# Performance work log

Measured on AMD Instinct MI355X. Metric: run time of the kernel, lower is better.

The kernel has to match this reference:

```python
import math
import jax, jax.numpy as jnp
import numpy as np

B, S, D = 1, 2048, 4096
H, KV, Dh = 32, 8, 128          # query heads, kv heads, head dim
G = H // KV                      # GQA group size
THETA = 10000.0
FACTOR = 4.0
BETA_FAST, BETA_SLOW, ORIG_MAX = 32, 1, 32768


def _yarn_rope_cache(seq_len):
    """YaRN-scaled RoPE cos/sin cache, matching YaRNRotaryEmbedding._build_cache."""
    inv_freq = 1.0 / (THETA ** (np.arange(0, Dh, 2, dtype=np.float32) / Dh))
    low = ORIG_MAX / (2 * math.pi * BETA_SLOW)
    high = ORIG_MAX / (2 * math.pi * BETA_FAST)
    freq = 1.0 / inv_freq
    smooth = np.clip((freq - low) / (high - low), 0.0, 1.0)
    inv_freq = (1.0 - smooth) * inv_freq + smooth * (inv_freq / FACTOR)
    t = np.arange(seq_len, dtype=np.float32)
    freqs = np.outer(t, inv_freq)                 # [S, Dh/2]
    emb = np.concatenate([freqs, freqs], axis=-1) # [S, Dh]
    return np.cos(emb).astype(np.float32), np.sin(emb).astype(np.float32)


def _rotate_half(x):
    x1, x2 = jnp.split(x, 2, axis=-1)
    return jnp.concatenate([-x2, x1], axis=-1)


def setup_inputs() -> dict:
    key = jax.random.key(0)
    k0, k1, k2, k3, k4 = jax.random.split(key, 5)
    scale = 0.02
    hidden_states = jax.random.normal(k0, (B, S, D), jnp.float32)
    Wq = jax.random.normal(k1, (H * Dh, D), jnp.float32) * scale
    Wk = jax.random.normal(k2, (KV * Dh, D), jnp.float32) * scale
    Wv = jax.random.normal(k3, (KV * Dh, D), jnp.float32) * scale
    Wo = jax.random.normal(k4, (D, H * Dh), jnp.float32) * scale
    cos_np, sin_np = _yarn_rope_cache(S)
    return {"hidden_states": hidden_states, "Wq": Wq, "Wk": Wk, "Wv": Wv,
            "Wo": Wo, "cos": jnp.asarray(cos_np), "sin": jnp.asarray(sin_np)}


def reference(hidden_states, Wq, Wk, Wv, Wo, cos, sin):
    x = hidden_states
    b, s, _ = x.shape
    # QKV projections (Linear, no bias): y = x @ W.T
    q = jnp.einsum('bsd,ed->bse', x, Wq).reshape(b, s, H, Dh).transpose(0, 2, 1, 3)   # [B,H,S,Dh]
    k = jnp.einsum('bsd,ed->bse', x, Wk).reshape(b, s, KV, Dh).transpose(0, 2, 1, 3)  # [B,KV,S,Dh]
    v = jnp.einsum('bsd,ed->bse', x, Wv).reshape(b, s, KV, Dh).transpose(0, 2, 1, 3)  # [B,KV,S,Dh]
    # YaRN RoPE (cos/sin: [S,Dh], broadcast over batch/head)
    c = cos[None, None, :, :]
    sn = sin[None, None, :, :]
    q = q * c + _rotate_half(q) * sn
    k = k * c + _rotate_half(k) * sn
    # GQA: group query heads over kv heads instead of materializing repeat_interleave
    qg = q.reshape(b, KV, G, s, Dh)
    scores = jnp.einsum('bkgqd,bknd->bkgqn', qg, k) / math.sqrt(Dh)  # [B,KV,G,S,S]
    causal = jnp.tril(jnp.ones((s, s), dtype=bool))
    scores = jnp.where(causal[None, None, None], scores, jnp.finfo(scores.dtype).min)
    w = jax.nn.softmax(scores.astype(jnp.float32), axis=-1).astype(x.dtype)
    attn = jnp.einsum('bkgqn,bknd->bkgqd', w, v)                      # [B,KV,G,S,Dh]
    attn = attn.reshape(b, H, s, Dh).transpose(0, 2, 1, 3).reshape(b, s, H * Dh)
    return jnp.einsum('bse,de->bsd', attn, Wo)
```

## Files before the change

kernel.cpp:

```cpp
#include <hip/hip_runtime.h>

#define S_LEN 2048
#define DMODEL 4096
#define NH 32
#define NKV 8
#define DH 128
#define QDIM (NH*DH)
#define NQKV 6144
#define SCALE 0.08838834764831845f

typedef __attribute__((ext_vector_type(8))) short short8;
typedef __attribute__((ext_vector_type(4))) float f32x4;
typedef __attribute__((ext_vector_type(4))) unsigned short us4;

__device__ __forceinline__ unsigned short f2bf(float f) {
  union { float f; unsigned int u; } v; v.f = f;
  unsigned int r = v.u + 0x7FFFu + ((v.u >> 16) & 1u);
  return (unsigned short)(r >> 16);
}
__device__ __forceinline__ float bf2f(unsigned short h) {
  union { unsigned int u; float f; } v; v.u = ((unsigned int)h) << 16;
  return v.f;
}

__global__ __launch_bounds__(256) void cvt_all(const float* __restrict__ x,
                                               const float* __restrict__ Wq,
                                               const float* __restrict__ Wk,
                                               const float* __restrict__ Wv,
                                               const float* __restrict__ Wo,
                                               unsigned short* __restrict__ xb,
                                               unsigned short* __restrict__ Wqkvb,
                                               unsigned short* __restrict__ Wob) {
  const int blk = blockIdx.x;
  const float* src; unsigned short* dst; int off;
  if (blk < 8192)       { src = x;  dst = xb;               off = blk; }
  else if (blk < 24576) { src = Wq; dst = Wqkvb;            off = blk - 8192; }
  else if (blk < 28672) { src = Wk; dst = Wqkvb + 16777216; off = blk - 24576; }
  else if (blk < 32768) { src = Wv; dst = Wqkvb + 20971520; off = blk - 28672; }
  else                  { src = Wo; dst = Wob;              off = blk - 32768; }
  int i = off * 256 + threadIdx.x;
  const float4 f = reinterpret_cast<const float4*>(src)[i];
  us4 o;
  o.x = f2bf(f.x); o.y = f2bf(f.y); o.z = f2bf(f.z); o.w = f2bf(f.w);
  reinterpret_cast<us4*>(dst)[i] = o;
}

template<int M_, int N_, int K_, int BM_, int BN_, int OUT_BF16, int CHN>
__global__ __launch_bounds__(512) void gemm8p(const unsigned short* __restrict__ A,
                                              const unsigned short* __restrict__ B,
                                              void* __restrict__ Cv) {
  constexpr int ATILE = BM_ * 128;
  constexpr int BTILE = BN_ * 128;
  constexpr int BUF = ATILE + BTILE;
  constexpr int LPA = BM_ / 64;
  constexpr int LPB = BN_ / 64;
  constexpr int VM  = LPA + LPB;
  constexpr int MI = BM_ / 32;
  constexpr int NF = BN_ / 64;
  constexpr int MIL = MI / 2;
  constexpr int NFL = NF / 2;
  constexpr int NT = K_ / 64;
  __shared__ char lds[2 * BUF];

  const int tid = threadIdx.x;
  const int lane = tid & 63, wave = tid >> 6;
  const int wm = wave >> 2, wn = wave & 3;
  const int fr = lane & 15, fq = lane >> 4;

  const int lin = blockIdx.x;
  const int xcd = lin & 7;
  const int slot = lin >> 3;
  const long n0 = (long)(xcd * CHN + slot % CHN) * BN_;
  const long m0 = (long)(slot / CHN) * BM_;

  auto STAGE_A = [&](int t, int c) {
#pragma unroll
    for (int u = 0; u < LPA; ++u) {
      int b = u * 8192 + tid * 16;
      int row = b >> 7;
      int off = (b & 127) ^ ((row & 7) << 4);
      __builtin_amdgcn_global_load_lds(
        (const __attribute__((address_space(1))) void*)((const char*)A + ((m0 + row) * (long)K_ + t * 64) * 2 + off),
        (__attribute__((address_space(3))) void*)(lds + c * BUF + b), 16, 0, 0);
    }
  };
  auto STAGE_B = [&](int t, int c) {
#pragma unroll
    for (int u = 0; u < LPB; ++u) {
      int b = u * 8192 + tid * 16;
      int row = b >> 7;
      int off = (b & 127) ^ ((row & 7) << 4);
      __builtin_amdgcn_global_load_lds(
        (const __attribute__((address_space(1))) void*)((const char*)B + ((n0 + row) * (long)K_ + t * 64) * 2 + off),
        (__attribute__((address_space(3))) void*)(lds + c * BUF + ATILE + b), 16, 0, 0);
    }
  };
#define VMCNT_STEADY() do { if constexpr (VM == 6) asm volatile("s_waitcnt vmcnt(6)" ::: "memory"); \
                            else if constexpr (VM == 7) asm volatile("s_waitcnt vmcnt(7)" ::: "memory"); \
                            else asm volatile("s_waitcnt vmcnt(8)" ::: "memory"); } while (0)

  f32x4 acc[MI][NF] = {};
  short8 af[MI][2];
  short8 bf[NF][2];

  STAGE_A(0, 0); STAGE_B(0, 0);
  STAGE_A(1, 1); STAGE_B(1, 1);
  VMCNT_STEADY();
  __builtin_amdgcn_s_barrier();

  for (int t = 0; t < NT; ++t) {
    const int c = t & 1;
    const char* tb = lds + c * BUF;

#pragma unroll
    for (int mi = 0; mi < MIL; ++mi) {
      int row = wm * (BM_ / 2) + mi * 16 + fr;
#pragma unroll
      for (int ks = 0; ks < 2; ++ks)
        af[mi][ks] = *(const short8*)(tb + row * 128 + ((ks * 64 + fq * 16) ^ ((row & 7) << 4)));
    }
#pragma unroll
    for (int ni = 0; ni < NFL; ++ni) {
      int row = wn * (BN_ / 4) + ni * 16 + fr;
#pragma unroll
      for (int ks = 0; ks < 2; ++ks)
        bf[ni][ks] = *(const short8*)(tb + ATILE + row * 128 + ((ks * 64 + fq * 16) ^ ((row & 7) << 4)));
    }
    __builtin_amdgcn_s_barrier();
    __builtin_amdgcn_s_setprio(1);
#pragma unroll
    for (int mi = 0; mi < MIL; ++mi)
#pragma unroll
      for (int ni = 0; ni < NFL; ++ni)
#pragma unroll
        for (int ks = 0; ks < 2; ++ks)
          acc[mi][ni] = __builtin_amdgcn_mfma_f32_16x16x32_bf16(af[mi][ks], bf[ni][ks], acc[mi][ni], 0, 0, 0);
    __builtin_amdgcn_s_setprio(0);
    __builtin_amdgcn_s_barrier();

#pragma unroll
    for (int mi = MIL; mi < MI; ++mi) {
      int row = wm * (BM_ / 2) + mi * 16 + fr;
#pragma unroll
      for (int ks = 0; ks < 2; ++ks)
        af[mi][ks] = *(const short8*)(tb + row * 128 + ((ks * 64 + fq * 16) ^ ((row & 7) << 4)));
    }
#pragma unroll
    for (int ni = NFL; ni < NF; ++ni) {
      int row = wn * (BN_ / 4) + ni * 16 + fr;
#pragma unroll
      for (int ks = 0; ks < 2; ++ks)
        bf[ni][ks] = *(const short8*)(tb + ATILE + row * 128 + ((ks * 64 + fq * 16) ^ ((row & 7) << 4)));
    }
    __builtin_amdgcn_s_barrier();
    __builtin_amdgcn_s_setprio(1);
#pragma unroll
    for (int mi = 0; mi < MIL; ++mi)
#pragma unroll
      for (int ni = NFL; ni < NF; ++ni)
#pragma unroll
        for (int ks = 0; ks < 2; ++ks)
          acc[mi][ni] = __builtin_amdgcn_mfma_f32_16x16x32_bf16(af[mi][ks], bf[ni][ks], acc[mi][ni], 0, 0, 0);
    __builtin_amdgcn_s_setprio(0);
    __builtin_amdgcn_s_barrier();

    if (t + 2 < NT) STAGE_A(t + 2, c);
    __builtin_amdgcn_s_setprio(1);
#pragma unroll
    for (int mi = MIL; mi < MI; ++mi)
#pragma unroll
      for (int ni = 0; ni < NFL; ++ni)
#pragma unroll
        for (int ks = 0; ks < 2; ++ks)
          acc[mi][ni] = __builtin_amdgcn_mfma_f32_16x16x32_bf16(af[mi][ks], bf[ni][ks], acc[mi][ni], 0, 0, 0);
    __builtin_amdgcn_s_setprio(0);
    __builtin_amdgcn_s_barrier();

    if (t + 2 < NT) STAGE_B(t + 2, c);
    __builtin_amdgcn_s_setprio(1);
#pragma unroll
    for (int mi = MIL; mi < MI; ++mi)
#pragma unroll
      for (int ni = NFL; ni < NF; ++ni)
#pragma unroll
        for (int ks = 0; ks < 2; ++ks)
          acc[mi][ni] = __builtin_amdgcn_mfma_f32_16x16x32_bf16(af[mi][ks], bf[ni][ks], acc[mi][ni], 0, 0, 0);
    __builtin_amdgcn_s_setprio(0);
    if (t + 2 < NT) { VMCNT_STEADY(); }
    else if (t + 1 < NT) { asm volatile("s_waitcnt vmcnt(0)" ::: "memory"); }
    __builtin_amdgcn_s_barrier();
  }
#undef VMCNT_STEADY

#pragma unroll
  for (int mi = 0; mi < MI; ++mi)
#pragma unroll
    for (int ni = 0; ni < NF; ++ni)
#pragma unroll
      for (int j = 0; j < 4; ++j) {
        long r = m0 + wm * (BM_ / 2) + mi * 16 + fq * 4 + j;
        long cc = n0 + wn * (BN_ / 4) + ni * 16 + fr;
        float v = acc[mi][ni][j];
        if (OUT_BF16) ((unsigned short*)Cv)[r * N_ + cc] = f2bf(v);
        else          ((float*)Cv)[r * N_ + cc] = v;
      }
}

__global__ __launch_bounds__(256) void rope_fused(unsigned short* __restrict__ C,
                                                  const float* __restrict__ cosb,
                                                  const float* __restrict__ sinb) {
  int idx = blockIdx.x * 256 + threadIdx.x;
  int i = idx & 63;
  int t = idx >> 6;
  int hh = t % 40;
  int s = t / 40;
  const bool isQ = hh < 32;
  unsigned short* row = C + (size_t)s * NQKV + (isQ ? hh * DH : 4096 + (hh - 32) * DH);
  float sc = isQ ? SCALE : 1.0f;
  float c  = cosb[s * DH + i];
  float sn = sinb[s * DH + i];
  float x1 = bf2f(row[i]);
  float x2 = bf2f(row[i + 64]);
  row[i]      = f2bf((x1 * c - x2 * sn) * sc);
  row[i + 64] = f2bf((x2 * c + x1 * sn) * sc);
}

__global__ __launch_bounds__(256) void transpose_v(const unsigned short* __restrict__ Vbuf,
                                                   unsigned short* __restrict__ VT) {
  __shared__ unsigned short t[64][72];
  const int s0 = blockIdx.x * 64, e0 = blockIdx.y * 64;
  const int r = threadIdx.x >> 3, c = (threadIdx.x & 7) * 8;
#pragma unroll
  for (int half = 0; half < 2; ++half) {
    int row = r + half * 32;
    *reinterpret_cast<short8*>(&t[row][c]) =
        *reinterpret_cast<const short8*>(Vbuf + (size_t)(s0 + row) * NQKV + e0 + c);
  }
  __syncthreads();
  const int hh = e0 >> 7, dbase = e0 & 127;
#pragma unroll
  for (int half = 0; half < 2; ++half) {
    int row = r + half * 32;
    short8 o;
#pragma unroll
    for (int j = 0; j < 8; ++j) ((unsigned short*)&o)[j] = t[c + j][row];
    *reinterpret_cast<short8*>(VT + (size_t)hh * (DH * (size_t)S_LEN)
                               + (size_t)(dbase + row) * S_LEN + s0 + c) = o;
  }
}

__global__ __launch_bounds__(256) void attn_fwd(const unsigned short* __restrict__ C,
                                                const unsigned short* __restrict__ VT,
                                                unsigned short* __restrict__ Ob) {
  __shared__ unsigned short KVs[2][8192];
  __shared__ unsigned short Pl[4][16 * 40];
  const int tid = threadIdx.x, lane = tid & 63, wave = tid >> 6;
  const int kvh = blockIdx.x & 7;
  const int p = blockIdx.x >> 3;
  const int h = kvh * 4 + wave;
  const int fr = lane & 15, fq = lane >> 4;
  const int q0s[2] = { p * 16, (127 - p) * 16 };
  const int tilesA = (p * 16 + 47) >> 5;
  const int tilesB = ((127 - p) * 16 + 47) >> 5;

  const unsigned short* Qbase = C + (size_t)h * DH;
  const unsigned short* Kbase = C + 4096 + (size_t)kvh * DH;
  const unsigned short* Vbase = VT + (size_t)kvh * (DH * (size_t)S_LEN);

  short8 qf[2][4];
#pragma unroll
  for (int s = 0; s < 2; ++s)
#pragma unroll
    for (int dc = 0; dc < 4; ++dc)
      qf[s][dc] = *reinterpret_cast<const short8*>(
          Qbase + (size_t)(q0s[s] + fr) * NQKV + dc * 32 + fq * 8);

  f32x4 o_acc[2][8] = {};
  float mrow[2][4] = {{-1e30f,-1e30f,-1e30f,-1e30f},{-1e30f,-1e30f,-1e30f,-1e30f}};
  float lpart[2][4] = {};

  auto STAGE = [&](int t, int buf) {
    const int kv0 = t * 32;
    char* dst = (char*)&KVs[buf][0];
#pragma unroll
    for (int sh = 0; sh < 2; ++sh) {
      int b = sh * 4096 + tid * 16;
      int krow = b >> 8;
      int kcol = (b & 255) ^ ((krow & 7) << 4);
      __builtin_amdgcn_global_load_lds(
          (const __attribute__((address_space(1))) void*)(Kbase + (size_t)(kv0 + krow) * NQKV + (kcol >> 1)),
          (__attribute__((address_space(3))) void*)(dst + b), 16, 0, 0);
      int vrow = b >> 6;
      int vcol = (b & 63) ^ ((((vrow ^ (vrow >> 2)) & 3)) << 4);
      __builtin_amdgcn_global_load_lds(
          (const __attribute__((address_space(1))) void*)(Vbase + (size_t)vrow * S_LEN + kv0 + (vcol >> 1)),
          (__attribute__((address_space(3))) void*)(dst + 8192 + b), 16, 0, 0);
    }
  };

  int cur = 0;
  STAGE(0, 0);
  asm volatile("s_waitcnt vmcnt(0)" ::: "memory");
  __syncthreads();

  for (int t = 0; t < tilesB; ++t) {
    const int kv0 = t * 32;
    if (t + 1 < tilesB) STAGE(t + 1, cur ^ 1);
    const char* kvb = (const char*)&KVs[cur][0];

#pragma unroll
    for (int s = 0; s < 2; ++s) {
      if (s == 0 && t >= tilesA) continue;
      const int q0 = q0s[s];

      f32x4 sacc[2] = {};
#pragma unroll
      for (int nt = 0; nt < 2; ++nt) {
        const int row = nt * 16 + fr;
#pragma unroll
        for (int dc = 0; dc < 4; ++dc) {
          short8 kf = *reinterpret_cast<const short8*>(
              kvb + row * 256 + ((dc * 64 + fq * 16) ^ ((row & 7) << 4)));
          sacc[nt] = __builtin_amdgcn_mfma_f32_16x16x32_bf16(qf[s][dc], kf, sacc[nt], 0, 0, 0);
        }
      }

      const bool needMask = (kv0 + 32 > q0);
      if (needMask) {
#pragma unroll
        for (int j = 0; j < 4; ++j) {
          int qrow = q0 + fq * 4 + j;
#pragma unroll
          for (int nt = 0; nt < 2; ++nt)
            sacc[nt][j] = ((kv0 + nt*16 + fr) <= qrow) ? sacc[nt][j] : -1e30f;
        }
      }
      bool ok = true;
      float lm[4];
#pragma unroll
      for (int j = 0; j < 4; ++j) {
        lm[j] = fmaxf(sacc[0][j], sacc[1][j]);
        ok = ok && (lm[j] <= mrow[s][j] + 8.f);
      }
      if (!__all(ok)) {
#pragma unroll
        for (int j = 0; j < 4; ++j) {
          float rm = lm[j];
          rm = fmaxf(rm, __shfl_xor(rm, 1));
          rm = fmaxf(rm, __shfl_xor(rm, 2));
          rm = fmaxf(rm, __shfl_xor(rm, 4));
          rm = fmaxf(rm, __shfl_xor(rm, 8));
          float mnew = fmaxf(mrow[s][j], rm);
          float corr = __expf(mrow[s][j] - mnew);
          mrow[s][j] = mnew;
          lpart[s][j] *= corr;
#pragma unroll
          for (int dt = 0; dt < 8; ++dt) o_acc[s][dt][j] *= corr;
        }
      }
#pragma unroll
      for (int j = 0; j < 4; ++j) {
        float p0 = __expf(sacc[0][j] - mrow[s][j]);
        float p1 = __expf(sacc[1][j] - mrow[s][j]);
        lpart[s][j] += p0 + p1;
        unsigned int u;
        asm("v_cvt_pk_bf16_f32 %0, %1, %2" : "=v"(u) : "v"(p0), "v"(p1));
        Pl[wave][(fq*4 + j)*40 + fr]      = (unsigned short)u;
        Pl[wave][(fq*4 + j)*40 + 16 + fr] = (unsigned short)(u >> 16);
      }
      asm volatile("s_waitcnt lgkmcnt(0)" ::: "memory");
      __builtin_amdgcn_sched_barrier(0);

      short8 pa = *reinterpret_cast<const short8*>(&Pl[wave][fr*40 + fq*8]);
#pragma unroll
      for (int dt = 0; dt < 8; ++dt) {
        const int row = dt * 16 + fr;
        short8 bv = *reinterpret_cast<const short8*>(
            kvb + 8192 + row * 64 + ((fq * 16) ^ ((((row ^ (row >> 2)) & 3)) << 4)));
        o_acc[s][dt] = __builtin_amdgcn_mfma_f32_16x16x32_bf16(pa, bv, o_acc[s][dt], 0, 0, 0);
      }
    }

    asm volatile("s_waitcnt vmcnt(0)" ::: "memory");
    __syncthreads();
    cur ^= 1;
  }

#pragma unroll
  for (int s = 0; s < 2; ++s)
#pragma unroll
    for (int j = 0; j < 4; ++j) {
      float l = lpart[s][j];
      l += __shfl_xor(l, 1);
      l += __shfl_xor(l, 2);
      l += __shfl_xor(l, 4);
      l += __shfl_xor(l, 8);
      float inv = 1.f / l;
      size_t r = (size_t)q0s[s] + fq*4 + j;
#pragma unroll
      for (int dt = 0; dt < 8; ++dt)
        Ob[r * QDIM + h * DH + dt*16 + fr] = f2bf(o_acc[s][dt][j] * inv);
    }
}

extern "C" void kernel_launch(void* const* d_in, const int* in_sizes, int n_in,
                              void* d_out, int out_size, void* d_ws, size_t ws_size,
                              hipStream_t stream) {
  (void)in_sizes; (void)n_in; (void)out_size; (void)ws_size;
  const float* x    = (const float*)d_in[0];
  const float* Wq   = (const float*)d_in[1];
  const float* Wk   = (const float*)d_in[2];
  const float* Wv   = (const float*)d_in[3];
  const float* Wo   = (const float*)d_in[4];
  const float* cosb = (const float*)d_in[5];
  const float* sinb = (const float*)d_in[6];

  char* ws = (char*)d_ws;
  unsigned short* xb    = (unsigned short*)(ws);
  unsigned short* Wqkvb = (unsigned short*)(ws + 16777216);
  unsigned short* Wob   = (unsigned short*)(ws + 67108864);
  unsigned short* Cqkv  = (unsigned short*)(ws + 100663296);
  unsigned short* VT    = (unsigned short*)(ws + 125829120);
  unsigned short* Ab    = xb;

  cvt_all<<<49152, 256, 0, stream>>>(x, Wq, Wk, Wv, Wo, xb, Wqkvb, Wob);

  gemm8p<2048, 6144, 4096, 256, 192, 1, 4><<<256, 512, 0, stream>>>(xb, Wqkvb, Cqkv);

  rope_fused<<<20480, 256, 0, stream>>>(Cqkv, cosb, sinb);
  transpose_v<<<dim3(32, 16), 256, 0, stream>>>(Cqkv + 5120, VT);

  attn_fwd<<<512, 256, 0, stream>>>(Cqkv, VT, Ab);

  gemm8p<2048, 4096, 4096, 128, 256, 0, 2><<<256, 512, 0, stream>>>(Ab, Wob, d_out);
}
```

Before: 306.2 us.

## Fuse fp32-to-bf16 weight conversion into GEMM B-tile loading

Removes the separate weight conversion pass. Both GEMMs now read fp32 weights directly into registers, convert them to bf16 with packed convert instructions and write them into the swizzled LDS tiles, with the Q/K/V rows selected by row ranges. This avoids writing and re-reading about 64MB of bf16 weights per call. In exchange the GEMM reads twice the bytes per B tile from fp32, and the B path uses register staging with full vmcnt(0) waits instead of asynchronous direct-to-LDS loads, which may stall the pipeline.

```diff
diff --git a/kernel.cpp b/kernel.cpp
--- a/kernel.cpp
+++ b/kernel.cpp
@@ -22,43 +22,39 @@
   union { unsigned int u; float f; } v; v.u = ((unsigned int)h) << 16;
   return v.f;
 }
-
-__global__ __launch_bounds__(256) void cvt_all(const float* __restrict__ x,
-                                               const float* __restrict__ Wq,
-                                               const float* __restrict__ Wk,
-                                               const float* __restrict__ Wv,
-                                               const float* __restrict__ Wo,
-                                               unsigned short* __restrict__ xb,
-                                               unsigned short* __restrict__ Wqkvb,
-                                               unsigned short* __restrict__ Wob) {
-  const int blk = blockIdx.x;
-  const float* src; unsigned short* dst; int off;
-  if (blk < 8192)       { src = x;  dst = xb;               off = blk; }
-  else if (blk < 24576) { src = Wq; dst = Wqkvb;            off = blk - 8192; }
-  else if (blk < 28672) { src = Wk; dst = Wqkvb + 16777216; off = blk - 24576; }
-  else if (blk < 32768) { src = Wv; dst = Wqkvb + 20971520; off = blk - 28672; }
-  else                  { src = Wo; dst = Wob;              off = blk - 32768; }
-  int i = off * 256 + threadIdx.x;
-  const float4 f = reinterpret_cast<const float4*>(src)[i];
+__device__ __forceinline__ short8 pack_bf16x8(float4 a, float4 b) {
+  unsigned int u0, u1, u2, u3;
+  asm("v_cvt_pk_bf16_f32 %0, %1, %2" : "=v"(u0) : "v"(a.x), "v"(a.y));
+  asm("v_cvt_pk_bf16_f32 %0, %1, %2" : "=v"(u1) : "v"(a.z), "v"(a.w));
+  asm("v_cvt_pk_bf16_f32 %0, %1, %2" : "=v"(u2) : "v"(b.x), "v"(b.y));
+  asm("v_cvt_pk_bf16_f32 %0, %1, %2" : "=v"(u3) : "v"(b.z), "v"(b.w));
+  union { unsigned int u[4]; short8 s; } r;
+  r.u[0] = u0; r.u[1] = u1; r.u[2] = u2; r.u[3] = u3;
+  return r.s;
+}
+
+__global__ __launch_bounds__(256) void cvt_x(const float* __restrict__ in,
+                                             unsigned short* __restrict__ out) {
+  int i = blockIdx.x * 256 + threadIdx.x;
+  const float4 f = reinterpret_cast<const float4*>(in)[i];
   us4 o;
   o.x = f2bf(f.x); o.y = f2bf(f.y); o.z = f2bf(f.z); o.w = f2bf(f.w);
-  reinterpret_cast<us4*>(dst)[i] = o;
-}
-
-template<int M_, int N_, int K_, int BM_, int BN_, int OUT_BF16, int CHN>
+  reinterpret_cast<us4*>(out)[i] = o;
+}
+
+template<int M_, int N_, int K_, int BM_, int BN_, int OUT_BF16, int CHN, int R1, int R2>
 __global__ __launch_bounds__(512) void gemm8p(const unsigned short* __restrict__ A,
-                                              const unsigned short* __restrict__ B,
+                                              const float* __restrict__ B0,
+                                              const float* __restrict__ B1,
+                                              const float* __restrict__ B2,
                                               void* __restrict__ Cv) {
   constexpr int ATILE = BM_ * 128;
   constexpr int BTILE = BN_ * 128;
   constexpr int BUF = ATILE + BTILE;
   constexpr int LPA = BM_ / 64;
   constexpr int LPB = BN_ / 64;
-  constexpr int VM  = LPA + LPB;
-  constexpr int MI = BM_ / 32;
-  constexpr int NF = BN_ / 64;
-  constexpr int MIL = MI / 2;
-  constexpr int NFL = NF / 2;
+  constexpr int MI = BM_ / 32, NF = BN_ / 64;
+  constexpr int MIL = MI / 2, NFL = NF / 2;
   constexpr int NT = K_ / 64;
   __shared__ char lds[2 * BUF];
 
@@ -73,6 +69,35 @@
   const long n0 = (long)(xcd * CHN + slot % CHN) * BN_;
   const long m0 = (long)(slot / CHN) * BM_;
 
+  const char* pB[LPB];
+  int bslot[LPB];
+#pragma unroll
+  for (int u = 0; u < LPB; ++u) {
+    int b = u * 8192 + tid * 16;
+    int row = b >> 7;
+    int colx = (b & 127) ^ ((row & 7) << 4);
+    long n = n0 + row;
+    const float* base = (n < R1) ? B0 + n * (long)K_
+                      : (n < R2) ? B1 + (n - R1) * (long)K_
+                                 : B2 + (n - (long)R2) * (long)K_;
+    pB[u] = (const char*)base + (long)colx * 2;
+    bslot[u] = b;
+  }
+  float4 breg[LPB][2];
+
+  auto B_ISSUE = [&](int t) {
+#pragma unroll
+    for (int u = 0; u < LPB; ++u) {
+      breg[u][0] = *reinterpret_cast<const float4*>(pB[u] + (long)t * 256);
+      breg[u][1] = *reinterpret_cast<const float4*>(pB[u] + (long)t * 256 + 16);
+    }
+  };
+  auto B_WRITE = [&](int c) {
+#pragma unroll
+    for (int u = 0; u < LPB; ++u)
+      *reinterpret_cast<short8*>(lds + c * BUF + ATILE + bslot[u]) =
+          pack_bf16x8(breg[u][0], breg[u][1]);
+  };
   auto STAGE_A = [&](int t, int c) {
 #pragma unroll
     for (int u = 0; u < LPA; ++u) {
@@ -84,28 +109,15 @@
         (__attribute__((address_space(3))) void*)(lds + c * BUF + b), 16, 0, 0);
     }
   };
-  auto STAGE_B = [&](int t, int c) {
-#pragma unroll
-    for (int u = 0; u < LPB; ++u) {
-      int b = u * 8192 + tid * 16;
-      int row = b >> 7;
-      int off = (b & 127) ^ ((row & 7) << 4);
-      __builtin_amdgcn_global_load_lds(
-        (const __attribute__((address_space(1))) void*)((const char*)B + ((n0 + row) * (long)K_ + t * 64) * 2 + off),
-        (__attribute__((address_space(3))) void*)(lds + c * BUF + ATILE + b), 16, 0, 0);
-    }
-  };
-#define VMCNT_STEADY() do { if constexpr (VM == 6) asm volatile("s_waitcnt vmcnt(6)" ::: "memory"); \
-                            else if constexpr (VM == 7) asm volatile("s_waitcnt vmcnt(7)" ::: "memory"); \
-                            else asm volatile("s_waitcnt vmcnt(8)" ::: "memory"); } while (0)
 
   f32x4 acc[MI][NF] = {};
   short8 af[MI][2];
   short8 bf[NF][2];
 
-  STAGE_A(0, 0); STAGE_B(0, 0);
-  STAGE_A(1, 1); STAGE_B(1, 1);
-  VMCNT_STEADY();
+  B_ISSUE(0); B_WRITE(0); STAGE_A(0, 0);
+  B_ISSUE(1); B_WRITE(1); STAGE_A(1, 1);
+  asm volatile("s_waitcnt vmcnt(0)" ::: "memory");
+  asm volatile("s_waitcnt lgkmcnt(0)" ::: "memory");
   __builtin_amdgcn_s_barrier();
 
   for (int t = 0; t < NT; ++t) {
@@ -126,6 +138,8 @@
       for (int ks = 0; ks < 2; ++ks)
         bf[ni][ks] = *(const short8*)(tb + ATILE + row * 128 + ((ks * 64 + fq * 16) ^ ((row & 7) << 4)));
     }
+    if (t + 2 < NT) B_ISSUE(t + 2);
+    __builtin_amdgcn_sched_barrier(0);
     __builtin_amdgcn_s_barrier();
     __builtin_amdgcn_s_setprio(1);
 #pragma unroll
@@ -164,7 +178,8 @@
     __builtin_amdgcn_s_setprio(0);
     __builtin_amdgcn_s_barrier();
 
-    if (t + 2 < NT) STAGE_A(t + 2, c);
+    asm volatile("s_waitcnt vmcnt(0)" ::: "memory");
+    if (t + 2 < NT) B_WRITE(c);
     __builtin_amdgcn_s_setprio(1);
 #pragma unroll
     for (int mi = MIL; mi < MI; ++mi)
@@ -176,7 +191,7 @@
     __builtin_amdgcn_s_setprio(0);
     __builtin_amdgcn_s_barrier();
 
-    if (t + 2 < NT) STAGE_B(t + 2, c);
+    if (t + 2 < NT) STAGE_A(t + 2, c);
     __builtin_amdgcn_s_setprio(1);
 #pragma unroll
     for (int mi = MIL; mi < MI; ++mi)
@@ -186,11 +201,9 @@
         for (int ks = 0; ks < 2; ++ks)
           acc[mi][ni] = __builtin_amdgcn_mfma_f32_16x16x32_bf16(af[mi][ks], bf[ni][ks], acc[mi][ni], 0, 0, 0);
     __builtin_amdgcn_s_setprio(0);
-    if (t + 2 < NT) { VMCNT_STEADY(); }
-    else if (t + 1 < NT) { asm volatile("s_waitcnt vmcnt(0)" ::: "memory"); }
+    asm volatile("s_waitcnt lgkmcnt(0)" ::: "memory");
     __builtin_amdgcn_s_barrier();
   }
-#undef VMCNT_STEADY
 
 #pragma unroll
   for (int mi = 0; mi < MI; ++mi)
@@ -417,20 +430,20 @@
 
   char* ws = (char*)d_ws;
   unsigned short* xb    = (unsigned short*)(ws);
-  unsigned short* Wqkvb = (unsigned short*)(ws + 16777216);
-  unsigned short* Wob   = (unsigned short*)(ws + 67108864);
   unsigned short* Cqkv  = (unsigned short*)(ws + 100663296);
   unsigned short* VT    = (unsigned short*)(ws + 125829120);
   unsigned short* Ab    = xb;
 
-  cvt_all<<<49152, 256, 0, stream>>>(x, Wq, Wk, Wv, Wo, xb, Wqkvb, Wob);
-
-  gemm8p<2048, 6144, 4096, 256, 192, 1, 4><<<256, 512, 0, stream>>>(xb, Wqkvb, Cqkv);
+  cvt_x<<<8192, 256, 0, stream>>>(x, xb);
+
+  gemm8p<2048, 6144, 4096, 256, 192, 1, 4, 4096, 5120>
+      <<<256, 512, 0, stream>>>(xb, Wq, Wk, Wv, Cqkv);
 
   rope_fused<<<20480, 256, 0, stream>>>(Cqkv, cosb, sinb);
   transpose_v<<<dim3(32, 16), 256, 0, stream>>>(Cqkv + 5120, VT);
 
   attn_fwd<<<512, 256, 0, stream>>>(Cqkv, VT, Ab);
 
-  gemm8p<2048, 4096, 4096, 128, 256, 0, 2><<<256, 512, 0, stream>>>(Ab, Wob, d_out);
-}
+  gemm8p<2048, 4096, 4096, 128, 256, 0, 2, (1 << 30), (1 << 30)>
+      <<<256, 512, 0, stream>>>(Ab, Wo, Wo, Wo, d_out);
+}
```

New measurement: 354.6 us. +15.8%, slower.

## Add triple-buffered LDS GEMM variant for output projection

Applied to the files above, without the earlier changes.

Adds gemm8p3, a copy of the GEMM kernel that uses three LDS buffers instead of two and prefetches two K-tiles ahead. The B-tile load for the future tile is split into halves and interleaved with the four MFMA quadrants. The output-projection GEMM now uses this variant. The aim is to hide global-load latency better, at the cost of more LDS per block, which may lower occupancy, and a hardcoded vmcnt wait count.

```diff
diff --git a/kernel.cpp b/kernel.cpp
--- a/kernel.cpp
+++ b/kernel.cpp
@@ -55,10 +55,8 @@
   constexpr int LPA = BM_ / 64;
   constexpr int LPB = BN_ / 64;
   constexpr int VM  = LPA + LPB;
-  constexpr int MI = BM_ / 32;
-  constexpr int NF = BN_ / 64;
-  constexpr int MIL = MI / 2;
-  constexpr int NFL = NF / 2;
+  constexpr int MI = BM_ / 32, NF = BN_ / 64;
+  constexpr int MIL = MI / 2, NFL = NF / 2;
   constexpr int NT = K_ / 64;
   __shared__ char lds[2 * BUF];
 
@@ -191,6 +189,163 @@
     __builtin_amdgcn_s_barrier();
   }
 #undef VMCNT_STEADY
+
+#pragma unroll
+  for (int mi = 0; mi < MI; ++mi)
+#pragma unroll
+    for (int ni = 0; ni < NF; ++ni)
+#pragma unroll
+      for (int j = 0; j < 4; ++j) {
+        long r = m0 + wm * (BM_ / 2) + mi * 16 + fq * 4 + j;
+        long cc = n0 + wn * (BN_ / 4) + ni * 16 + fr;
+        float v = acc[mi][ni][j];
+        if (OUT_BF16) ((unsigned short*)Cv)[r * N_ + cc] = f2bf(v);
+        else          ((float*)Cv)[r * N_ + cc] = v;
+      }
+}
+
+template<int M_, int N_, int K_, int BM_, int BN_, int OUT_BF16, int CHN>
+__global__ __launch_bounds__(512) void gemm8p3(const unsigned short* __restrict__ A,
+                                               const unsigned short* __restrict__ B,
+                                               void* __restrict__ Cv) {
+  constexpr int ATILE = BM_ * 128;
+  constexpr int BTILE = BN_ * 128;
+  constexpr int BUF = ATILE + BTILE;
+  constexpr int LPA = BM_ / 64;
+  constexpr int LPB = BN_ / 64;
+  constexpr int VM  = LPA + LPB;
+  constexpr int MI = BM_ / 32, NF = BN_ / 64;
+  constexpr int MIL = MI / 2, NFL = NF / 2;
+  constexpr int NT = K_ / 64;
+  __shared__ char lds[3 * BUF];
+
+  const int tid = threadIdx.x;
+  const int lane = tid & 63, wave = tid >> 6;
+  const int wm = wave >> 2, wn = wave & 3;
+  const int fr = lane & 15, fq = lane >> 4;
+
+  const int lin = blockIdx.x;
+  const int xcd = lin & 7;
+  const int slot = lin >> 3;
+  const long n0 = (long)(xcd * CHN + slot % CHN) * BN_;
+  const long m0 = (long)(slot / CHN) * BM_;
+
+  auto STAGE_A = [&](int t, int c) {
+#pragma unroll
+    for (int u = 0; u < LPA; ++u) {
+      int b = u * 8192 + tid * 16;
+      int row = b >> 7;
+      int off = (b & 127) ^ ((row & 7) << 4);
+      __builtin_amdgcn_global_load_lds(
+        (const __attribute__((address_space(1))) void*)((const char*)A + ((m0 + row) * (long)K_ + t * 64) * 2 + off),
+        (__attribute__((address_space(3))) void*)(lds + c * BUF + b), 16, 0, 0);
+    }
+  };
+  auto STAGE_B_HALF = [&](int t, int c, int half) {
+#pragma unroll
+    for (int u = 0; u < LPB / 2; ++u) {
+      int b = (half * (LPB / 2) + u) * 8192 + tid * 16;
+      int row = b >> 7;
+      int off = (b & 127) ^ ((row & 7) << 4);
+      __builtin_amdgcn_global_load_lds(
+        (const __attribute__((address_space(1))) void*)((const char*)B + ((n0 + row) * (long)K_ + t * 64) * 2 + off),
+        (__attribute__((address_space(3))) void*)(lds + c * BUF + ATILE + b), 16, 0, 0);
+    }
+  };
+
+  f32x4 acc[MI][NF] = {};
+  short8 af[MI][2];
+  short8 bf[NF][2];
+
+  STAGE_A(0, 0); STAGE_B_HALF(0, 0, 0); STAGE_B_HALF(0, 0, 1);
+  STAGE_A(1, 1); STAGE_B_HALF(1, 1, 0); STAGE_B_HALF(1, 1, 1);
+  asm volatile("s_waitcnt vmcnt(0)" ::: "memory");
+  __builtin_amdgcn_s_barrier();
+
+  for (int t = 0; t < NT; ++t) {
+    const char* tb = lds + (t % 3) * BUF;
+    const int c2 = (t + 2) % 3;
+
+#pragma unroll
+    for (int mi = 0; mi < MIL; ++mi) {
+      int row = wm * (BM_ / 2) + mi * 16 + fr;
+#pragma unroll
+      for (int ks = 0; ks < 2; ++ks)
+        af[mi][ks] = *(const short8*)(tb + row * 128 + ((ks * 64 + fq * 16) ^ ((row & 7) << 4)));
+    }
+#pragma unroll
+    for (int ni = 0; ni < NFL; ++ni) {
+      int row = wn * (BN_ / 4) + ni * 16 + fr;
+#pragma unroll
+      for (int ks = 0; ks < 2; ++ks)
+        bf[ni][ks] = *(const short8*)(tb + ATILE + row * 128 + ((ks * 64 + fq * 16) ^ ((row & 7) << 4)));
+    }
+    if (t + 2 < NT) STAGE_A(t + 2, c2);
+    __builtin_amdgcn_s_barrier();
+    __builtin_amdgcn_s_setprio(1);
+#pragma unroll
+    for (int mi = 0; mi < MIL; ++mi)
+#pragma unroll
+      for (int ni = 0; ni < NFL; ++ni)
+#pragma unroll
+        for (int ks = 0; ks < 2; ++ks)
+          acc[mi][ni] = __builtin_amdgcn_mfma_f32_16x16x32_bf16(af[mi][ks], bf[ni][ks], acc[mi][ni], 0, 0, 0);
+    __builtin_amdgcn_s_setprio(0);
+    __builtin_amdgcn_s_barrier();
+
+#pragma unroll
+    for (int mi = MIL; mi < MI; ++mi) {
+      int row = wm * (BM_ / 2) + mi * 16 + fr;
+#pragma unroll
+      for (int ks = 0; ks < 2; ++ks)
+        af[mi][ks] = *(const short8*)(tb + row * 128 + ((ks * 64 + fq * 16) ^ ((row & 7) << 4)));
+    }
+#pragma unroll
+    for (int ni = NFL; ni < NF; ++ni) {
+      int row = wn * (BN_ / 4) + ni * 16 + fr;
+#pragma unroll
+      for (int ks = 0; ks < 2; ++ks)
+        bf[ni][ks] = *(const short8*)(tb + ATILE + row * 128 + ((ks * 64 + fq * 16) ^ ((row & 7) << 4)));
+    }
+    if (t + 2 < NT) STAGE_B_HALF(t + 2, c2, 0);
+    __builtin_amdgcn_s_barrier();
+    __builtin_amdgcn_s_setprio(1);
+#pragma unroll
+    for (int mi = 0; mi < MIL; ++mi)
+#pragma unroll
+      for (int ni = NFL; ni < NF; ++ni)
+#pragma unroll
+        for (int ks = 0; ks < 2; ++ks)
+          acc[mi][ni] = __builtin_amdgcn_mfma_f32_16x16x32_bf16(af[mi][ks], bf[ni][ks], acc[mi][ni], 0, 0, 0);
+    __builtin_amdgcn_s_setprio(0);
+    __builtin_amdgcn_s_barrier();
+
+    if (t + 2 < NT) STAGE_B_HALF(t + 2, c2, 1);
+    __builtin_amdgcn_s_setprio(1);
+#pragma unroll
+    for (int mi = MIL; mi < MI; ++mi)
+#pragma unroll
+      for (int ni = 0; ni < NFL; ++ni)
+#pragma unroll
+        for (int ks = 0; ks < 2; ++ks)
+          acc[mi][ni] = __builtin_amdgcn_mfma_f32_16x16x32_bf16(af[mi][ks], bf[ni][ks], acc[mi][ni], 0, 0, 0);
+    __builtin_amdgcn_s_setprio(0);
+    __builtin_amdgcn_s_barrier();
+
+    __builtin_amdgcn_s_setprio(1);
+#pragma unroll
+    for (int mi = MIL; mi < MI; ++mi)
+#pragma unroll
+      for (int ni = NFL; ni < NF; ++ni)
+#pragma unroll
+        for (int ks = 0; ks < 2; ++ks)
+          acc[mi][ni] = __builtin_amdgcn_mfma_f32_16x16x32_bf16(af[mi][ks], bf[ni][ks], acc[mi][ni], 0, 0, 0);
+    __builtin_amdgcn_s_setprio(0);
+    if (t + 2 < NT) { asm volatile("s_waitcnt vmcnt(6)" ::: "memory"); }
+    else if (t + 1 < NT) { asm volatile("s_waitcnt vmcnt(0)" ::: "memory"); }
+    __builtin_amdgcn_s_barrier();
+  }
+  (void)VM;
 
 #pragma unroll
   for (int mi = 0; mi < MI; ++mi)
@@ -432,5 +587,5 @@
 
   attn_fwd<<<512, 256, 0, stream>>>(Cqkv, VT, Ab);
 
-  gemm8p<2048, 4096, 4096, 128, 256, 0, 2><<<256, 512, 0, stream>>>(Ab, Wob, d_out);
-}
+  gemm8p3<2048, 4096, 4096, 128, 256, 0, 2><<<256, 512, 0, stream>>>(Ab, Wob, d_out);
+}
```

New measurement: 306.0 us. About the same (-0.1%).

## Fuse Q RoPE and Wo conversion into attention, merge K RoPE with V transpose

Applied to the files above, without the earlier changes.

Moves the Wo fp32-to-bf16 conversion into the attention kernel, where each block converts a slice per KV tile and so hides the conversion under attention compute. Applies Q RoPE and scaling in registers after loading the Q fragments instead of in a separate pass. Merges K RoPE and the V transpose into one launch. Regroups the GEMM inner loop into four M-row groups with all B fragments loaded up front. Together these cut kernel launches and global round trips, at the cost of more registers in both the attention and GEMM kernels.

```diff
diff --git a/kernel.cpp b/kernel.cpp
--- a/kernel.cpp
+++ b/kernel.cpp
@@ -27,17 +27,14 @@
                                                const float* __restrict__ Wq,
                                                const float* __restrict__ Wk,
                                                const float* __restrict__ Wv,
-                                               const float* __restrict__ Wo,
                                                unsigned short* __restrict__ xb,
-                                               unsigned short* __restrict__ Wqkvb,
-                                               unsigned short* __restrict__ Wob) {
+                                               unsigned short* __restrict__ Wqkvb) {
   const int blk = blockIdx.x;
   const float* src; unsigned short* dst; int off;
   if (blk < 8192)       { src = x;  dst = xb;               off = blk; }
   else if (blk < 24576) { src = Wq; dst = Wqkvb;            off = blk - 8192; }
   else if (blk < 28672) { src = Wk; dst = Wqkvb + 16777216; off = blk - 24576; }
-  else if (blk < 32768) { src = Wv; dst = Wqkvb + 20971520; off = blk - 28672; }
-  else                  { src = Wo; dst = Wob;              off = blk - 32768; }
+  else                  { src = Wv; dst = Wqkvb + 20971520; off = blk - 28672; }
   int i = off * 256 + threadIdx.x;
   const float4 f = reinterpret_cast<const float4*>(src)[i];
   us4 o;
@@ -55,10 +52,8 @@
   constexpr int LPA = BM_ / 64;
   constexpr int LPB = BN_ / 64;
   constexpr int VM  = LPA + LPB;
-  constexpr int MI = BM_ / 32;
-  constexpr int NF = BN_ / 64;
-  constexpr int MIL = MI / 2;
-  constexpr int NFL = NF / 2;
+  constexpr int MI = BM_ / 32, NF = BN_ / 64;
+  constexpr int MG = MI / 4;
   constexpr int NT = K_ / 64;
   __shared__ char lds[2 * BUF];
 
@@ -98,6 +93,17 @@
 #define VMCNT_STEADY() do { if constexpr (VM == 6) asm volatile("s_waitcnt vmcnt(6)" ::: "memory"); \
                             else if constexpr (VM == 7) asm volatile("s_waitcnt vmcnt(7)" ::: "memory"); \
                             else asm volatile("s_waitcnt vmcnt(8)" ::: "memory"); } while (0)
+#define MFMA_GROUP(g) do { \
+  __builtin_amdgcn_s_setprio(1); \
+  _Pragma("unroll") \
+  for (int mi = (g) * MG; mi < ((g) + 1) * MG; ++mi) \
+    _Pragma("unroll") \
+    for (int ni = 0; ni < NF; ++ni) \
+      _Pragma("unroll") \
+      for (int ks = 0; ks < 2; ++ks) \
+        acc[mi][ni] = __builtin_amdgcn_mfma_f32_16x16x32_bf16(af[mi][ks], bf[ni][ks], acc[mi][ni], 0, 0, 0); \
+  __builtin_amdgcn_s_setprio(0); \
+} while (0)
 
   f32x4 acc[MI][NF] = {};
   short8 af[MI][2];
@@ -113,84 +119,46 @@
     const char* tb = lds + c * BUF;
 
 #pragma unroll
-    for (int mi = 0; mi < MIL; ++mi) {
+    for (int mi = 0; mi < 2 * MG; ++mi) {
       int row = wm * (BM_ / 2) + mi * 16 + fr;
 #pragma unroll
       for (int ks = 0; ks < 2; ++ks)
         af[mi][ks] = *(const short8*)(tb + row * 128 + ((ks * 64 + fq * 16) ^ ((row & 7) << 4)));
     }
 #pragma unroll
-    for (int ni = 0; ni < NFL; ++ni) {
+    for (int ni = 0; ni < NF; ++ni) {
       int row = wn * (BN_ / 4) + ni * 16 + fr;
 #pragma unroll
       for (int ks = 0; ks < 2; ++ks)
         bf[ni][ks] = *(const short8*)(tb + ATILE + row * 128 + ((ks * 64 + fq * 16) ^ ((row & 7) << 4)));
     }
     __builtin_amdgcn_s_barrier();
-    __builtin_amdgcn_s_setprio(1);
-#pragma unroll
-    for (int mi = 0; mi < MIL; ++mi)
-#pragma unroll
-      for (int ni = 0; ni < NFL; ++ni)
-#pragma unroll
-        for (int ks = 0; ks < 2; ++ks)
-          acc[mi][ni] = __builtin_amdgcn_mfma_f32_16x16x32_bf16(af[mi][ks], bf[ni][ks], acc[mi][ni], 0, 0, 0);
-    __builtin_amdgcn_s_setprio(0);
-    __builtin_amdgcn_s_barrier();
-
-#pragma unroll
-    for (int mi = MIL; mi < MI; ++mi) {
+    MFMA_GROUP(0);
+    __builtin_amdgcn_s_barrier();
+
+#pragma unroll
+    for (int mi = 2 * MG; mi < 4 * MG; ++mi) {
       int row = wm * (BM_ / 2) + mi * 16 + fr;
 #pragma unroll
       for (int ks = 0; ks < 2; ++ks)
         af[mi][ks] = *(const short8*)(tb + row * 128 + ((ks * 64 + fq * 16) ^ ((row & 7) << 4)));
     }
-#pragma unroll
-    for (int ni = NFL; ni < NF; ++ni) {
-      int row = wn * (BN_ / 4) + ni * 16 + fr;
-#pragma unroll
-      for (int ks = 0; ks < 2; ++ks)
-        bf[ni][ks] = *(const short8*)(tb + ATILE + row * 128 + ((ks * 64 + fq * 16) ^ ((row & 7) << 4)));
-    }
-    __builtin_amdgcn_s_barrier();
-    __builtin_amdgcn_s_setprio(1);
-#pragma unroll
-    for (int mi = 0; mi < MIL; ++mi)
-#pragma unroll
-      for (int ni = NFL; ni < NF; ++ni)
-#pragma unroll
-        for (int ks = 0; ks < 2; ++ks)
-          acc[mi][ni] = __builtin_amdgcn_mfma_f32_16x16x32_bf16(af[mi][ks], bf[ni][ks], acc[mi][ni], 0, 0, 0);
-    __builtin_amdgcn_s_setprio(0);
+    __builtin_amdgcn_s_barrier();
+    MFMA_GROUP(1);
     __builtin_amdgcn_s_barrier();
 
     if (t + 2 < NT) STAGE_A(t + 2, c);
-    __builtin_amdgcn_s_setprio(1);
-#pragma unroll
-    for (int mi = MIL; mi < MI; ++mi)
-#pragma unroll
-      for (int ni = 0; ni < NFL; ++ni)
-#pragma unroll
-        for (int ks = 0; ks < 2; ++ks)
-          acc[mi][ni] = __builtin_amdgcn_mfma_f32_16x16x32_bf16(af[mi][ks], bf[ni][ks], acc[mi][ni], 0, 0, 0);
-    __builtin_amdgcn_s_setprio(0);
+    MFMA_GROUP(2);
     __builtin_amdgcn_s_barrier();
 
     if (t + 2 < NT) STAGE_B(t + 2, c);
-    __builtin_amdgcn_s_setprio(1);
-#pragma unroll
-    for (int mi = MIL; mi < MI; ++mi)
-#pragma unroll
-      for (int ni = NFL; ni < NF; ++ni)
-#pragma unroll
-        for (int ks = 0; ks < 2; ++ks)
-          acc[mi][ni] = __builtin_amdgcn_mfma_f32_16x16x32_bf16(af[mi][ks], bf[ni][ks], acc[mi][ni], 0, 0, 0);
-    __builtin_amdgcn_s_setprio(0);
+    MFMA_GROUP(3);
     if (t + 2 < NT) { VMCNT_STEADY(); }
     else if (t + 1 < NT) { asm volatile("s_waitcnt vmcnt(0)" ::: "memory"); }
     __builtin_amdgcn_s_barrier();
   }
 #undef VMCNT_STEADY
+#undef MFMA_GROUP
 
 #pragma unroll
   for (int mi = 0; mi < MI; ++mi)
@@ -206,34 +174,35 @@
       }
 }
 
-__global__ __launch_bounds__(256) void rope_fused(unsigned short* __restrict__ C,
-                                                  const float* __restrict__ cosb,
-                                                  const float* __restrict__ sinb) {
-  int idx = blockIdx.x * 256 + threadIdx.x;
-  int i = idx & 63;
-  int t = idx >> 6;
-  int hh = t % 40;
-  int s = t / 40;
-  const bool isQ = hh < 32;
-  unsigned short* row = C + (size_t)s * NQKV + (isQ ? hh * DH : 4096 + (hh - 32) * DH);
-  float sc = isQ ? SCALE : 1.0f;
-  float c  = cosb[s * DH + i];
-  float sn = sinb[s * DH + i];
-  float x1 = bf2f(row[i]);
-  float x2 = bf2f(row[i + 64]);
-  row[i]      = f2bf((x1 * c - x2 * sn) * sc);
-  row[i + 64] = f2bf((x2 * c + x1 * sn) * sc);
-}
-
-__global__ __launch_bounds__(256) void transpose_v(const unsigned short* __restrict__ Vbuf,
-                                                   unsigned short* __restrict__ VT) {
-  __shared__ unsigned short t[64][72];
-  const int s0 = blockIdx.x * 64, e0 = blockIdx.y * 64;
+__global__ __launch_bounds__(256) void ropek_tv(unsigned short* __restrict__ C,
+                                                const float* __restrict__ cosb,
+                                                const float* __restrict__ sinb,
+                                                unsigned short* __restrict__ VT) {
+  __shared__ unsigned short tbuf[64][72];
+  const int blk = blockIdx.x;
+  if (blk < 4096) {
+    int idx = blk * 256 + threadIdx.x;
+    int i = idx & 63;
+    int t = idx >> 6;
+    int hh = t & 7;
+    int s = t >> 3;
+    unsigned short* row = C + (size_t)s * NQKV + 4096 + hh * DH;
+    float c  = cosb[s * DH + i];
+    float sn = sinb[s * DH + i];
+    float x1 = bf2f(row[i]);
+    float x2 = bf2f(row[i + 64]);
+    row[i]      = f2bf(x1 * c - x2 * sn);
+    row[i + 64] = f2bf(x2 * c + x1 * sn);
+    return;
+  }
+  const int b2 = blk - 4096;
+  const unsigned short* Vbuf = C + 5120;
+  const int s0 = (b2 & 31) * 64, e0 = (b2 >> 5) * 64;
   const int r = threadIdx.x >> 3, c = (threadIdx.x & 7) * 8;
 #pragma unroll
   for (int half = 0; half < 2; ++half) {
     int row = r + half * 32;
-    *reinterpret_cast<short8*>(&t[row][c]) =
+    *reinterpret_cast<short8*>(&tbuf[row][c]) =
         *reinterpret_cast<const short8*>(Vbuf + (size_t)(s0 + row) * NQKV + e0 + c);
   }
   __syncthreads();
@@ -243,7 +212,7 @@
     int row = r + half * 32;
     short8 o;
 #pragma unroll
-    for (int j = 0; j < 8; ++j) ((unsigned short*)&o)[j] = t[c + j][row];
+    for (int j = 0; j < 8; ++j) ((unsigned short*)&o)[j] = tbuf[c + j][row];
     *reinterpret_cast<short8*>(VT + (size_t)hh * (DH * (size_t)S_LEN)
                                + (size_t)(dbase + row) * S_LEN + s0 + c) = o;
   }
@@ -251,7 +220,11 @@
 
 __global__ __launch_bounds__(256) void attn_fwd(const unsigned short* __restrict__ C,
                                                 const unsigned short* __restrict__ VT,
-                                                unsigned short* __restrict__ Ob) {
+                                                unsigned short* __restrict__ Ob,
+                                                const float* __restrict__ Wo,
+                                                unsigned short* __restrict__ Wob,
+                                                const float* __restrict__ cosb,
+                                                const float* __restrict__ sinb) {
   __shared__ unsigned short KVs[2][8192];
   __shared__ unsigned short Pl[4][16 * 40];
   const int tid = threadIdx.x, lane = tid & 63, wave = tid >> 6;
@@ -267,6 +240,9 @@
   const unsigned short* Kbase = C + 4096 + (size_t)kvh * DH;
   const unsigned short* Vbase = VT + (size_t)kvh * (DH * (size_t)S_LEN);
 
+  const int wq0 = blockIdx.x * 8192 + tid;
+  float4 wreg;
+
   short8 qf[2][4];
 #pragma unroll
   for (int s = 0; s < 2; ++s)
@@ -274,6 +250,23 @@
     for (int dc = 0; dc < 4; ++dc)
       qf[s][dc] = *reinterpret_cast<const short8*>(
           Qbase + (size_t)(q0s[s] + fr) * NQKV + dc * 32 + fq * 8);
+
+#pragma unroll
+  for (int s = 0; s < 2; ++s) {
+    const int row = q0s[s] + fr;
+#pragma unroll
+    for (int dc = 0; dc < 2; ++dc)
+#pragma unroll
+      for (int e = 0; e < 8; ++e) {
+        int d = dc * 32 + fq * 8 + e;
+        float cs = cosb[row * DH + d];
+        float sn = sinb[row * DH + d];
+        float x1 = bf2f((unsigned short)qf[s][dc][e]);
+        float x2 = bf2f((unsigned short)qf[s][dc + 2][e]);
+        qf[s][dc][e]     = (short)f2bf((x1 * cs - x2 * sn) * SCALE);
+        qf[s][dc + 2][e] = (short)f2bf((x2 * cs + x1 * sn) * SCALE);
+      }
+  }
 
   f32x4 o_acc[2][8] = {};
   float mrow[2][4] = {{-1e30f,-1e30f,-1e30f,-1e30f},{-1e30f,-1e30f,-1e30f,-1e30f}};
@@ -305,6 +298,14 @@
 
   for (int t = 0; t < tilesB; ++t) {
     const int kv0 = t * 32;
+
+    if (t > 0 && t <= 32) {
+      us4 o;
+      o.x = f2bf(wreg.x); o.y = f2bf(wreg.y); o.z = f2bf(wreg.z); o.w = f2bf(wreg.w);
+      reinterpret_cast<us4*>(Wob)[wq0 + (t - 1) * 256] = o;
+    }
+    if (t < 32) wreg = reinterpret_cast<const float4*>(Wo)[wq0 + t * 256];
+
     if (t + 1 < tilesB) STAGE(t + 1, cur ^ 1);
     const char* kvb = (const char*)&KVs[cur][0];
 
@@ -423,14 +424,13 @@
   unsigned short* VT    = (unsigned short*)(ws + 125829120);
   unsigned short* Ab    = xb;
 
-  cvt_all<<<49152, 256, 0, stream>>>(x, Wq, Wk, Wv, Wo, xb, Wqkvb, Wob);
+  cvt_all<<<32768, 256, 0, stream>>>(x, Wq, Wk, Wv, xb, Wqkvb);
 
   gemm8p<2048, 6144, 4096, 256, 192, 1, 4><<<256, 512, 0, stream>>>(xb, Wqkvb, Cqkv);
 
-  rope_fused<<<20480, 256, 0, stream>>>(Cqkv, cosb, sinb);
-  transpose_v<<<dim3(32, 16), 256, 0, stream>>>(Cqkv + 5120, VT);
-
-  attn_fwd<<<512, 256, 0, stream>>>(Cqkv, VT, Ab);
+  ropek_tv<<<4608, 256, 0, stream>>>(Cqkv, cosb, sinb, VT);
+
+  attn_fwd<<<512, 256, 0, stream>>>(Cqkv, VT, Ab, Wo, Wob, cosb, sinb);
 
   gemm8p<2048, 4096, 4096, 128, 256, 0, 2><<<256, 512, 0, stream>>>(Ab, Wob, d_out);
 }
```

Measured after the change: 290.7 us. 5.1% less time.
